# Performance work log

Hardware: AMD Instinct MI355X
Metric: run time of the kernel (lower is better)

The kernel has to match this reference:

```python
import jax, jax.numpy as jnp
import numpy as np

B, N, OUTERDIM, DIM, N_CLASSES = 2, 6000, 1024, 512, 2
HEADS, DIM_HEAD, INNER = 8, 64, 512
LANDMARKS, PINV_ITERS, KPAD = 256, 6, 16  # residual conv kernel 33 -> pad 16
SCALE = DIM_HEAD ** -0.5


def layer_norm(x, g, b, eps=1e-5):
    mu = x.mean(-1, keepdims=True)
    var = jnp.var(x, axis=-1, keepdims=True)
    return (x - mu) * jax.lax.rsqrt(var + eps) * g + b


def moore_penrose_pinv(x, iters=PINV_ITERS):
    # x: [b, h, m, m]
    abs_x = jnp.abs(x)
    col = abs_x.sum(-1)
    row = abs_x.sum(-2)
    z = jnp.swapaxes(x, -1, -2) / (jnp.max(col) * jnp.max(row))
    I = jnp.eye(x.shape[-1], dtype=x.dtype)
    for _ in range(iters):
        xz = x @ z
        z = 0.25 * z @ (13 * I - xz @ (15 * I - xz @ (7 * I - xz)))
    return z


def nystrom_attention(x, w_qkv, w_out, b_out, conv_w):
    b, n, _ = x.shape
    pad = (-n) % LANDMARKS
    xp = jnp.pad(x, ((0, 0), (pad, 0), (0, 0)))  # pad at FRONT, as in lucidrains impl
    npad = n + pad
    qkv = xp @ w_qkv.T  # [b, npad, 3*inner]
    q, k, v = [t.reshape(b, npad, HEADS, DIM_HEAD).transpose(0, 2, 1, 3)
               for t in jnp.split(qkv, 3, axis=-1)]
    q = q * SCALE
    l = npad // LANDMARKS  # tokens per landmark
    q_l = q.reshape(b, HEADS, LANDMARKS, l, DIM_HEAD).sum(3) / l
    k_l = k.reshape(b, HEADS, LANDMARKS, l, DIM_HEAD).sum(3) / l
    attn1 = jax.nn.softmax(jnp.einsum('bhid,bhjd->bhij', q, k_l), axis=-1)   # [b,h,npad,m]
    attn2 = jax.nn.softmax(jnp.einsum('bhid,bhjd->bhij', q_l, k_l), axis=-1)  # [b,h,m,m]
    attn3 = jax.nn.softmax(jnp.einsum('bhid,bhjd->bhij', q_l, k), axis=-1)    # [b,h,m,npad]
    out = (attn1 @ moore_penrose_pinv(attn2)) @ (attn3 @ v)  # [b,h,npad,d]
    # depthwise residual conv over sequence dim (per head), kernel (33,1)
    out = out + jax.lax.conv_general_dilated(
        v, conv_w, window_strides=(1, 1), padding=((KPAD, KPAD), (0, 0)),
        dimension_numbers=('NCHW', 'OIHW', 'NCHW'), feature_group_count=HEADS)
    out = out.transpose(0, 2, 1, 3).reshape(b, npad, INNER)
    out = out @ w_out.T + b_out
    return out[:, -n:]


def setup_inputs() -> dict:
    key = jax.random.key(0)
    ks = jax.random.split(key, 12)
    w = lambda k, shape: 0.02 * jax.random.normal(k, shape, dtype=jnp.float32)
    inp = {
        'data': jax.random.normal(ks[0], (B, N, OUTERDIM), dtype=jnp.float32),
        'w1': w(ks[1], (DIM, OUTERDIM)), 'b1': jnp.zeros((DIM,), jnp.float32),
        'cls_token': jax.random.normal(ks[2], (1, 1, DIM), dtype=jnp.float32),
        'ln1_g': jnp.ones((DIM,), jnp.float32), 'ln1_b': jnp.zeros((DIM,), jnp.float32),
        'qkv1_w': w(ks[3], (3 * INNER, DIM)),
        'out1_w': w(ks[4], (DIM, INNER)), 'out1_b': jnp.zeros((DIM,), jnp.float32),
        'conv1_w': w(ks[5], (HEADS, 1, 33, 1)),
        'ln2_g': jnp.ones((DIM,), jnp.float32), 'ln2_b': jnp.zeros((DIM,), jnp.float32),
        'qkv2_w': w(ks[6], (3 * INNER, DIM)),
        'out2_w': w(ks[7], (DIM, INNER)), 'out2_b': jnp.zeros((DIM,), jnp.float32),
        'conv2_w': w(ks[8], (HEADS, 1, 33, 1)),
        'lnf_g': jnp.ones((DIM,), jnp.float32), 'lnf_b': jnp.zeros((DIM,), jnp.float32),
        'w2': w(ks[9], (N_CLASSES, DIM)), 'b2': jnp.zeros((N_CLASSES,), jnp.float32),
    }
    return inp


def reference(data, w1, b1, cls_token, ln1_g, ln1_b, qkv1_w, out1_w, out1_b, conv1_w,
              ln2_g, ln2_b, qkv2_w, out2_w, out2_b, conv2_w, lnf_g, lnf_b, w2, b2):
    h = jax.nn.relu(data @ w1.T + b1)  # [B, N, DIM]
    H = h.shape[1]
    side = int(np.ceil(np.sqrt(H)))
    add = side * side - H
    h = jnp.concatenate([h, h[:, :add]], axis=1)  # square padding: 6084
    cls = jnp.broadcast_to(cls_token, (h.shape[0], 1, h.shape[2]))
    h = jnp.concatenate([cls, h], axis=1)  # +CLS: 6085
    h = h + nystrom_attention(layer_norm(h, ln1_g, ln1_b), qkv1_w, out1_w, out1_b, conv1_w)
    h = h + nystrom_attention(layer_norm(h, ln2_g, ln2_b), qkv2_w, out2_w, out2_b, conv2_w)
    h = layer_norm(h, lnf_g, lnf_b)[:, 0]
    logits = h @ w2.T + b2
    return logits
```

## Files before the change

kernel.cpp:

```cpp
#include <hip/hip_runtime.h>
#include <cstdint>
#include <cstddef>

namespace {

constexpr int DIMC  = 512;
constexpr int SEQ   = 6085;
constexpr int NPAD  = 6144;
constexpr int PADF  = 59;
constexpr int LMK   = 256;
constexpr int BHN   = 16;
constexpr int KSPL  = 16;
constexpr int MPADR = 6016;

typedef __attribute__((ext_vector_type(8))) short bf8_t;
typedef __attribute__((ext_vector_type(4))) float f4_t;

#define SWZB(r, cu) (((((r) << 6) + ((cu) << 1))) ^ (((r) & 7) << 4))

#define GLDS16(gp, lp) __builtin_amdgcn_global_load_lds( \
    (const __attribute__((address_space(1))) void*)(gp), \
    (__attribute__((address_space(3))) void*)(lp), 16, 0, 0)

__device__ __forceinline__ ushort f2bf(float f) {
    union { float f; uint32_t u; } c{f};
    uint32_t u = c.u;
    return (ushort)((u + 0x7FFFu + ((u >> 16) & 1u)) >> 16);
}
__device__ __forceinline__ float bf2f(ushort u) {
    union { uint32_t u; float f; } c{(uint32_t)u << 16};
    return c.f;
}

__device__ __forceinline__ float waveSum(float v) {
#pragma unroll
    for (int o = 32; o > 0; o >>= 1) v += __shfl_xor(v, o, 64);
    return v;
}
__device__ __forceinline__ float waveMax(float v) {
#pragma unroll
    for (int o = 32; o > 0; o >>= 1) v = fmaxf(v, __shfl_xor(v, o, 64));
    return v;
}
__device__ __forceinline__ float blockSum256(float v, float* sm) {
    v = waveSum(v);
    __syncthreads();
    if ((threadIdx.x & 63) == 0) sm[threadIdx.x >> 6] = v;
    __syncthreads();
    return sm[0] + sm[1] + sm[2] + sm[3];
}
__device__ __forceinline__ float blockMax256(float v, float* sm) {
    v = waveMax(v);
    __syncthreads();
    if ((threadIdx.x & 63) == 0) sm[threadIdx.x >> 6] = v;
    __syncthreads();
    return fmaxf(fmaxf(sm[0], sm[1]), fmaxf(sm[2], sm[3]));
}

template<int EPI>
__global__ __launch_bounds__(256)
void gemm_bt(const ushort* __restrict__ A, const ushort* __restrict__ B,
             void* __restrict__ Cv, int M, int N, int K,
             int lda, int ldb, int ldc,
             long long sA, long long sB, long long sC,
             const float* __restrict__ bias, int relu,
             ushort* __restrict__ qp, ushort* __restrict__ kp, ushort* __restrict__ vp)
{
    __shared__ __align__(16) char As_s[128 * 128];
    __shared__ __align__(16) char Bs_s[128 * 128];
    const int z = blockIdx.z;
    const ushort* Ab = A + (size_t)z * sA;
    const ushort* Bb = B + (size_t)z * sB;
    const int row0 = blockIdx.y * 128, col0 = blockIdx.x * 128;
    const int tid = threadIdx.x, wid = tid >> 6, lane = tid & 63;
    const int wr = wid >> 1, wc = wid & 1, lr = lane & 15, kg = lane >> 4;
    const int srow = lane >> 3, sq = lane & 7;
    f4_t acc[4][4] = {};
    for (int k0 = 0; k0 < K; k0 += 64) {
        __syncthreads();
#pragma unroll
        for (int i = 0; i < 4; ++i) {
            int r = wid * 32 + i * 8 + srow;
            int qs = sq ^ (r & 7);
            GLDS16(Ab + (size_t)(row0 + r) * lda + k0 + qs * 8,
                   As_s + (wid * 32 + i * 8) * 128);
        }
#pragma unroll
        for (int i = 0; i < 4; ++i) {
            int r = wid * 32 + i * 8 + srow;
            int qs = sq ^ (r & 7);
            GLDS16(Bb + (size_t)(col0 + r) * ldb + k0 + qs * 8,
                   Bs_s + (wid * 32 + i * 8) * 128);
        }
        asm volatile("s_waitcnt vmcnt(0)" ::: "memory");
        __syncthreads();
#pragma unroll
        for (int ks = 0; ks < 2; ++ks) {
            bf8_t af[4], bg[4];
#pragma unroll
            for (int mr = 0; mr < 4; ++mr) {
                int r = wr * 64 + mr * 16 + lr;
                af[mr] = *(const bf8_t*)(As_s + r * 128 + ((((ks << 2) | kg) ^ (r & 7)) << 4));
            }
#pragma unroll
            for (int nr = 0; nr < 4; ++nr) {
                int r = wc * 64 + nr * 16 + lr;
                bg[nr] = *(const bf8_t*)(Bs_s + r * 128 + ((((ks << 2) | kg) ^ (r & 7)) << 4));
            }
#pragma unroll
            for (int mr = 0; mr < 4; ++mr)
#pragma unroll
                for (int nr = 0; nr < 4; ++nr)
                    acc[mr][nr] = __builtin_amdgcn_mfma_f32_16x16x32_bf16(af[mr], bg[nr], acc[mr][nr], 0, 0, 0);
        }
    }
#pragma unroll
    for (int mr = 0; mr < 4; ++mr) {
#pragma unroll
        for (int nr = 0; nr < 4; ++nr) {
#pragma unroll
            for (int r = 0; r < 4; ++r) {
                int gm = row0 + wr * 64 + mr * 16 + kg * 4 + r;
                int gn = col0 + wc * 64 + nr * 16 + lr;
                if (gm >= M || gn >= N) continue;
                float val = acc[mr][nr][r];
                if (EPI == 0) {
                    if (bias) val += bias[gn];
                    if (relu) val = fmaxf(val, 0.f);
                    ((float*)Cv)[(size_t)z * sC + (size_t)gm * ldc + gn] = val;
                } else if (EPI == 1) {
                    ((ushort*)Cv)[(size_t)z * sC + (size_t)gm * ldc + gn] = f2bf(val);
                } else {
                    int b = (gm >= NPAD) ? 1 : 0;
                    int i = gm - b * NPAD;
                    int which = gn >> 9, hh = (gn >> 6) & 7, d = gn & 63;
                    size_t dst = ((size_t)(b * 8 + hh) * NPAD + i) * 64 + d;
                    if (which == 0)      qp[dst] = f2bf(val * 0.125f);
                    else if (which == 1) kp[dst] = f2bf(val);
                    else                 vp[dst] = f2bf(val);
                }
            }
        }
    }
}

__global__ __launch_bounds__(256)
void attn1_fused(const ushort* __restrict__ q, const ushort* __restrict__ kl,
                 const ushort* __restrict__ Wt, ushort* __restrict__ ot)
{
    __shared__ __align__(16) char P_s[128 * 512];
    const int mt = blockIdx.x;
    const int bh = blockIdx.y;
    const int b = bh >> 3, hh = bh & 7;
    const int tid = threadIdx.x, wid = tid >> 6, lane = tid & 63;
    const int lr = lane & 15, kg = lane >> 4;
    const int row0 = mt * 128;
    const ushort* qb  = q  + (size_t)bh * NPAD * 64;
    const ushort* klb = kl + (size_t)bh * LMK * 64;
    const ushort* Wtb = Wt + (size_t)bh * 128 * 256;

    f4_t acc[2][16];
#pragma unroll
    for (int mf = 0; mf < 2; ++mf)
#pragma unroll
        for (int nf = 0; nf < 16; ++nf) acc[mf][nf] = (f4_t){0.f, 0.f, 0.f, 0.f};
#pragma unroll
    for (int ks = 0; ks < 2; ++ks) {
        bf8_t af[2];
#pragma unroll
        for (int mf = 0; mf < 2; ++mf)
            af[mf] = *(const bf8_t*)&qb[(size_t)(row0 + wid * 32 + mf * 16 + lr) * 64 + ks * 32 + kg * 8];
#pragma unroll
        for (int nf = 0; nf < 16; ++nf) {
            bf8_t bg = *(const bf8_t*)&klb[(size_t)(nf * 16 + lr) * 64 + ks * 32 + kg * 8];
            acc[0][nf] = __builtin_amdgcn_mfma_f32_16x16x32_bf16(af[0], bg, acc[0][nf], 0, 0, 0);
            acc[1][nf] = __builtin_amdgcn_mfma_f32_16x16x32_bf16(af[1], bg, acc[1][nf], 0, 0, 0);
        }
    }
    float inv_s[2][4];
#pragma unroll
    for (int mf = 0; mf < 2; ++mf) {
        float mx[4] = {-1e30f, -1e30f, -1e30f, -1e30f};
#pragma unroll
        for (int nf = 0; nf < 16; ++nf)
#pragma unroll
            for (int r = 0; r < 4; ++r) mx[r] = fmaxf(mx[r], acc[mf][nf][r]);
#pragma unroll
        for (int r = 0; r < 4; ++r) {
            mx[r] = fmaxf(mx[r], __shfl_xor(mx[r], 1, 64));
            mx[r] = fmaxf(mx[r], __shfl_xor(mx[r], 2, 64));
            mx[r] = fmaxf(mx[r], __shfl_xor(mx[r], 4, 64));
            mx[r] = fmaxf(mx[r], __shfl_xor(mx[r], 8, 64));
        }
        float sum[4] = {0.f, 0.f, 0.f, 0.f};
        const int rowb = wid * 32 + mf * 16 + kg * 4;
        const int cc2 = (lr & 7) * 2;
        const int chi = lr >> 3;
#pragma unroll
        for (int nf = 0; nf < 16; ++nf) {
#pragma unroll
            for (int r = 0; r < 4; ++r) {
                float e = expf(acc[mf][nf][r] - mx[r]);
                sum[r] += e;
                int row = rowb + r;
                int chunk = (2 * nf + chi) ^ (row & 7);
                *(ushort*)(P_s + row * 512 + chunk * 16 + cc2) = f2bf(e);
            }
        }
#pragma unroll
        for (int r = 0; r < 4; ++r) {
            sum[r] += __shfl_xor(sum[r], 1, 64);
            sum[r] += __shfl_xor(sum[r], 2, 64);
            sum[r] += __shfl_xor(sum[r], 4, 64);
            sum[r] += __shfl_xor(sum[r], 8, 64);
            inv_s[mf][r] = 1.f / sum[r];
        }
    }
    f4_t acc2[2][4] = {};
#pragma unroll
    for (int kt = 0; kt < 8; ++kt) {
        bf8_t af2[2];
#pragma unroll
        for (int mf = 0; mf < 2; ++mf) {
            int row = wid * 32 + mf * 16 + lr;
            int chunk = (kt * 4 + kg) ^ (row & 7);
            af2[mf] = *(const bf8_t*)(P_s + row * 512 + chunk * 16);
        }
#pragma unroll
        for (int nf = 0; nf < 4; ++nf) {
            bf8_t bg = *(const bf8_t*)&Wtb[(size_t)(nf * 16 + lr) * 256 + kt * 32 + kg * 8];
            acc2[0][nf] = __builtin_amdgcn_mfma_f32_16x16x32_bf16(af2[0], bg, acc2[0][nf], 0, 0, 0);
            acc2[1][nf] = __builtin_amdgcn_mfma_f32_16x16x32_bf16(af2[1], bg, acc2[1][nf], 0, 0, 0);
        }
    }
#pragma unroll
    for (int mf = 0; mf < 2; ++mf)
#pragma unroll
        for (int nf = 0; nf < 4; ++nf)
#pragma unroll
            for (int r = 0; r < 4; ++r) {
                int gm = row0 + wid * 32 + mf * 16 + kg * 4 + r;
                int gn = nf * 16 + lr;
                ot[((size_t)(b * NPAD + gm)) * DIMC + hh * 64 + gn] =
                    f2bf(acc2[mf][nf][r] * inv_s[mf][r]);
            }
}

__global__ __launch_bounds__(256)
void gemm_ns(const ushort* __restrict__ A, const ushort* __restrict__ B,
             ushort* __restrict__ C, ushort* __restrict__ C2, ushort* __restrict__ CT,
             float alpha, float c2d, int K, int N,
             long long sA, long long sB, long long sC, long long sCT)
{
    __shared__ __align__(16) char As_s[64 * 64];
    __shared__ __align__(16) char Bs_s[64 * 64];
    const int z = blockIdx.z;
    const int row0 = blockIdx.y * 64, col0 = blockIdx.x * 64;
    const int tid = threadIdx.x;
    const int wid = tid >> 6, lane = tid & 63;
    const int lr = lane & 15, kg = lane >> 4;
    const ushort* Ab = A + (size_t)z * sA;
    const ushort* Bb = B + (size_t)z * sB;
    f4_t acc[4] = {};
    const int am = tid >> 2, ac8 = (tid & 3) * 8;
    for (int k0 = 0; k0 < K; k0 += 32) {
        *(bf8_t*)(As_s + SWZB(am, ac8)) = *(const bf8_t*)&Ab[(size_t)(row0 + am) * K + k0 + ac8];
#pragma unroll
        for (int p = 0; p < 8; ++p) {
            int kk = p * 4 + (tid >> 6), n = tid & 63;
            *(ushort*)(Bs_s + SWZB(n, kk)) = Bb[(size_t)(k0 + kk) * N + col0 + n];
        }
        __syncthreads();
        bf8_t af = *(const bf8_t*)(As_s + SWZB(wid * 16 + lr, kg * 8));
#pragma unroll
        for (int j = 0; j < 4; ++j) {
            bf8_t bg = *(const bf8_t*)(Bs_s + SWZB(j * 16 + lr, kg * 8));
            acc[j] = __builtin_amdgcn_mfma_f32_16x16x32_bf16(af, bg, acc[j], 0, 0, 0);
        }
        __syncthreads();
    }
#pragma unroll
    for (int j = 0; j < 4; ++j) {
#pragma unroll
        for (int r = 0; r < 4; ++r) {
            int gm = row0 + wid * 16 + kg * 4 + r;
            int gn = col0 + j * 16 + lr;
            float val = alpha * acc[j][r];
            if (C)  C[(size_t)z * sC + (size_t)gm * N + gn] = f2bf(val);
            if (C2) C2[(size_t)z * sC + (size_t)gm * N + gn] = f2bf(((gm == gn) ? c2d : 0.f) - val);
            if (CT) CT[(size_t)z * sCT + (size_t)gn * LMK + gm] = f2bf(val);
        }
    }
}

__global__ __launch_bounds__(256)
void pv_splitk(const ushort* __restrict__ S, const ushort* __restrict__ v,
               float* __restrict__ o2p)
{
    __shared__ __align__(16) char As_s[128 * 64];
    __shared__ __align__(16) char Bs_s[64 * 64];
    const int split = blockIdx.x, mt = blockIdx.y, bh = blockIdx.z;
    const int tid = threadIdx.x;
    const int wid = tid >> 6, lane = tid & 63;
    const int lr = lane & 15, kg = lane >> 4;
    const ushort* Sb = S + (size_t)bh * LMK * NPAD + (size_t)(mt * 128) * NPAD;
    const ushort* vb = v + (size_t)bh * NPAD * 64;
    const int ks0 = split * (NPAD / KSPL);
    f4_t acc[2][4] = {};
    for (int k0 = ks0; k0 < ks0 + NPAD / KSPL; k0 += 32) {
#pragma unroll
        for (int p = 0; p < 2; ++p) {
            int idx = p * 256 + tid;
            int m = idx >> 2, kc = (idx & 3) * 8;
            *(bf8_t*)(As_s + SWZB(m, kc)) = *(const bf8_t*)&Sb[(size_t)m * NPAD + k0 + kc];
        }
#pragma unroll
        for (int p = 0; p < 8; ++p) {
            int kk = p * 4 + (tid >> 6), n = tid & 63;
            *(ushort*)(Bs_s + SWZB(n, kk)) = vb[(size_t)(k0 + kk) * 64 + n];
        }
        __syncthreads();
        bf8_t af[2], bg[4];
#pragma unroll
        for (int i = 0; i < 2; ++i)
            af[i] = *(const bf8_t*)(As_s + SWZB(wid * 32 + i * 16 + lr, kg * 8));
#pragma unroll
        for (int j = 0; j < 4; ++j)
            bg[j] = *(const bf8_t*)(Bs_s + SWZB(j * 16 + lr, kg * 8));
#pragma unroll
        for (int i = 0; i < 2; ++i)
#pragma unroll
            for (int j = 0; j < 4; ++j)
                acc[i][j] = __builtin_amdgcn_mfma_f32_16x16x32_bf16(af[i], bg[j], acc[i][j], 0, 0, 0);
        __syncthreads();
    }
#pragma unroll
    for (int i = 0; i < 2; ++i)
#pragma unroll
        for (int j = 0; j < 4; ++j)
#pragma unroll
            for (int r = 0; r < 4; ++r) {
                int gm = mt * 128 + wid * 32 + i * 16 + kg * 4 + r;
                int gn = j * 16 + lr;
                o2p[((size_t)(split * BHN + bh) * LMK + gm) * 64 + gn] = acc[i][j][r];
            }
}

__global__ void reduce_o2(const float* __restrict__ o2p, ushort* __restrict__ o2) {
    int idx = blockIdx.x * 256 + threadIdx.x;
    int bh = idx >> 14, e = idx & 16383;
    float s = 0.f;
#pragma unroll
    for (int sp = 0; sp < KSPL; ++sp)
        s += o2p[((size_t)(sp * BHN + bh) << 14) + e];
    o2[idx] = f2bf(s);
}

__global__ void cvt_bf16(const float* __restrict__ in, ushort* __restrict__ out, int n8) {
    int i = blockIdx.x * 256 + threadIdx.x;
    if (i >= n8) return;
    float4 a = ((const float4*)in)[i * 2], b = ((const float4*)in)[i * 2 + 1];
    ushort4 lo = { f2bf(a.x), f2bf(a.y), f2bf(a.z), f2bf(a.w) };
    ushort4 hi = { f2bf(b.x), f2bf(b.y), f2bf(b.z), f2bf(b.w) };
    ((ushort4*)out)[i * 2] = lo;
    ((ushort4*)out)[i * 2 + 1] = hi;
}

__global__ void extend_h(float* __restrict__ h, const float* __restrict__ cls) {
    int b = blockIdx.y, bx = blockIdx.x;
    float* hb = h + (size_t)b * SEQ * DIMC;
    for (int c = threadIdx.x; c < DIMC; c += 256) {
        if (bx == 0) hb[c] = cls[c];
        else hb[(size_t)(6000 + bx) * DIMC + c] = hb[(size_t)bx * DIMC + c];
    }
}

__global__ void zero_xp_pad(ushort* __restrict__ xp) {
    int e = blockIdx.x * 256 + threadIdx.x;
    int b = e / (PADF * DIMC);
    int rest = e - b * (PADF * DIMC);
    xp[(size_t)b * NPAD * DIMC + rest] = 0;
}

__global__ __launch_bounds__(128)
void ln_to_xp(const float* __restrict__ h, const float* __restrict__ g,
              const float* __restrict__ bb, ushort* __restrict__ xp)
{
    __shared__ float sm[2];
    int r = blockIdx.x;
    int b = r / SEQ, i = r - b * SEQ;
    int t = threadIdx.x;
    const float4* row = (const float4*)(h + (size_t)r * DIMC);
    float4 x = row[t];
    float s  = x.x + x.y + x.z + x.w;
    float sq = x.x * x.x + x.y * x.y + x.z * x.z + x.w * x.w;
    s = waveSum(s);
    sq = waveSum(sq);
    int w = t >> 6;
    if ((t & 63) == 0) sm[w] = s;
    __syncthreads();
    float S = sm[0] + sm[1];
    __syncthreads();
    if ((t & 63) == 0) sm[w] = sq;
    __syncthreads();
    float SQ = sm[0] + sm[1];
    float mu = S * (1.f / DIMC);
    float var = SQ * (1.f / DIMC) - mu * mu;
    float rs = rsqrtf(var + 1e-5f);
    float4 gg = ((const float4*)g)[t];
    float4 bv = ((const float4*)bb)[t];
    ushort4 o;
    o.x = f2bf((x.x - mu) * rs * gg.x + bv.x);
    o.y = f2bf((x.y - mu) * rs * gg.y + bv.y);
    o.z = f2bf((x.z - mu) * rs * gg.z + bv.z);
    o.w = f2bf((x.w - mu) * rs * gg.w + bv.w);
    ((ushort4*)(xp + ((size_t)b * NPAD + PADF + i) * DIMC))[t] = o;
}

__global__ void landmark_mean(const ushort* __restrict__ in, ushort* __restrict__ out) {
    int m = blockIdx.x, bh = blockIdx.y, d = threadIdx.x;
    const ushort* p = in + ((size_t)bh * NPAD + (size_t)m * (NPAD / LMK)) * 64 + d;
    float s = 0.f;
#pragma unroll
    for (int j = 0; j < NPAD / LMK; ++j) s += bf2f(p[(size_t)j * 64]);
    out[((size_t)bh * LMK + m) * 64 + d] = f2bf(s * (1.f / (NPAD / LMK)));
}

__global__ __launch_bounds__(256)
void softmax_bf_wide(ushort* __restrict__ S) {
    __shared__ float sm[4];
    ushort* p = S + (size_t)blockIdx.x * NPAD;
    int t = threadIdx.x;
    float v[24];
    float mx = -1e30f;
#pragma unroll
    for (int j = 0; j < 24; ++j) { v[j] = bf2f(p[j * 256 + t]); mx = fmaxf(mx, v[j]); }
    float bm = blockMax256(mx, sm);
    float s = 0.f;
#pragma unroll
    for (int j = 0; j < 24; ++j) { v[j] = expf(v[j] - bm); s += v[j]; }
    float bs = blockSum256(s, sm);
    float inv = 1.f / bs;
#pragma unroll
    for (int j = 0; j < 24; ++j) p[j * 256 + t] = f2bf(v[j] * inv);
}

__global__ __launch_bounds__(256)
void softmax_bf256(ushort* __restrict__ S) {
    __shared__ float sm[4];
    ushort* p = S + (size_t)blockIdx.x * 256;
    int t = threadIdx.x;
    float v = bf2f(p[t]);
    float bm = blockMax256(v, sm);
    float e = expf(v - bm);
    float bs = blockSum256(e, sm);
    p[t] = f2bf(e / bs);
}

__global__ __launch_bounds__(256)
void colsum_max(const ushort* __restrict__ X, float* __restrict__ scal) {
    __shared__ float sm[4];
    int bh = blockIdx.x, t = threadIdx.x;
    const ushort* Xb = X + ((size_t)bh << 16);
    float s = 0.f;
#pragma unroll 8
    for (int i = 0; i < 256; ++i) s += bf2f(Xb[(size_t)i * 256 + t]);
    float m = blockMax256(s, sm);
    if (t == 0) atomicMax((unsigned int*)scal, __float_as_uint(m));
}

__global__ void init_z(const ushort* __restrict__ X, const float* __restrict__ scal,
                       ushort* __restrict__ Z) {
    size_t e = (size_t)blockIdx.x * 256 + threadIdx.x;
    int c = (int)(e & 255);
    int r = (int)((e >> 8) & 255);
    size_t bh = e >> 16;
    float inv = 1.f / scal[0];
    Z[e] = f2bf(bf2f(X[(bh << 16) + (size_t)c * 256 + r]) * inv);
}

__global__ __launch_bounds__(256)
void conv_add(const ushort* __restrict__ v, const float* __restrict__ cw,
              ushort* __restrict__ ot)
{
    __shared__ float w[33];
    __shared__ ushort vt[96][64];
    int bh = blockIdx.y;
    int b = bh >> 3, hh = bh & 7;
    int i0 = blockIdx.x * 64;
    int t = threadIdx.x;
    if (t < 33) w[t] = cw[hh * 33 + t];
    const ushort* vb = v + (size_t)bh * NPAD * 64;
    int d = t & 63;
    for (int rr = t >> 6; rr < 96; rr += 4) {
        int j = i0 - 16 + rr;
        vt[rr][d] = (j >= 0 && j < NPAD) ? vb[(size_t)j * 64 + d] : (ushort)0;
    }
    __syncthreads();
    for (int ii = t >> 6; ii < 64; ii += 4) {
        float acc = 0.f;
#pragma unroll
        for (int kk = 0; kk < 33; ++kk) acc += w[kk] * bf2f(vt[ii + kk][d]);
        size_t off = ((size_t)(b * NPAD + i0 + ii)) * DIMC + hh * 64 + d;
        ot[off] = f2bf(bf2f(ot[off]) + acc);
    }
}

__global__ void residual_add(float* __restrict__ h, const float* __restrict__ y) {
    size_t e = (size_t)blockIdx.x * 256 + threadIdx.x;
    int c = (int)(e & 511);
    size_t ri = e >> 9;
    int i = (int)(ri % SEQ);
    int b = (int)(ri / SEQ);
    h[e] += y[((size_t)b * NPAD + PADF + i) * DIMC + c];
}

__global__ __launch_bounds__(256)
void final_head(const float* __restrict__ h, const float* __restrict__ g,
                const float* __restrict__ bb, const float* __restrict__ w2,
                const float* __restrict__ b2, float* __restrict__ out)
{
    __shared__ float row[DIMC];
    __shared__ float sm[4];
    int b = blockIdx.x;
    int t = threadIdx.x;
    const float* x = h + (size_t)b * SEQ * DIMC;
    float v0 = x[t], v1 = x[t + 256];
    float S = blockSum256(v0 + v1, sm);
    float SQ = blockSum256(v0 * v0 + v1 * v1, sm);
    float mu = S * (1.f / DIMC);
    float rs = rsqrtf(SQ * (1.f / DIMC) - mu * mu + 1e-5f);
    row[t] = (v0 - mu) * rs * g[t] + bb[t];
    row[t + 256] = (v1 - mu) * rs * g[t + 256] + bb[t + 256];
    __syncthreads();
    if (t < 64) {
        float a0 = 0.f, a1 = 0.f;
        for (int idx = t; idx < DIMC; idx += 64) {
            a0 += row[idx] * w2[idx];
            a1 += row[idx] * w2[DIMC + idx];
        }
        a0 = waveSum(a0);
        a1 = waveSum(a1);
        if (t == 0) {
            out[b * 2 + 0] = a0 + b2[0];
            out[b * 2 + 1] = a1 + b2[1];
        }
    }
}

void bt(int epi, const ushort* A, const ushort* B, void* C, int M, int N, int K,
        int lda, int ldb, int ldc, long long sA, long long sB, long long sC, int batch,
        const float* bias, int relu, ushort* qp, ushort* kp, ushort* vp, hipStream_t s)
{
    dim3 g((N + 127) / 128, (M + 127) / 128, batch), blk(256);
    switch (epi) {
    case 0: gemm_bt<0><<<g, blk, 0, s>>>(A, B, C, M, N, K, lda, ldb, ldc, sA, sB, sC, bias, relu, qp, kp, vp); break;
    case 1: gemm_bt<1><<<g, blk, 0, s>>>(A, B, C, M, N, K, lda, ldb, ldc, sA, sB, sC, bias, relu, qp, kp, vp); break;
    default: gemm_bt<2><<<g, blk, 0, s>>>(A, B, C, M, N, K, lda, ldb, ldc, sA, sB, sC, bias, relu, qp, kp, vp); break;
    }
}

void ns(const ushort* A, const ushort* B, ushort* C, ushort* C2, ushort* CT,
        float alpha, float c2d, int M, int N, int K,
        long long sA, long long sB, long long sC, long long sCT, hipStream_t s)
{
    dim3 g(N / 64, M / 64, BHN), blk(256);
    gemm_ns<<<g, blk, 0, s>>>(A, B, C, C2, CT, alpha, c2d, K, N, sA, sB, sC, sCT);
}

struct WS {
    float *h, *scal, *o2p, *y;
    ushort *xp, *q, *k, *v, *ql, *kl;
    ushort *datab, *w1b, *qkvwb1, *qkvwb2, *outwb1, *outwb2;
    ushort *X, *Z0, *Z1, *XZ, *TA, *TB, *TC;
    ushort *o2b, *Wt, *S, *ot;
};

void nystrom_layer(float* h, const float* lng, const float* lnb,
                   const ushort* qkvwb, const ushort* outwb, const float* outb,
                   const float* convw, const WS& w, hipStream_t s)
{
    const long long SM = (long long)LMK * LMK;
    zero_xp_pad<<<(2 * PADF * DIMC) / 256, 256, 0, s>>>(w.xp);
    ln_to_xp<<<2 * SEQ, 128, 0, s>>>(h, lng, lnb, w.xp);
    bt(2, w.xp, qkvwb, nullptr, 2 * NPAD, 3 * DIMC, DIMC, DIMC, DIMC, 0,
       0, 0, 0, 1, nullptr, 0, w.q, w.k, w.v, s);
    landmark_mean<<<dim3(LMK, BHN), 64, 0, s>>>(w.q, w.ql);
    landmark_mean<<<dim3(LMK, BHN), 64, 0, s>>>(w.k, w.kl);
    bt(1, w.ql, w.kl, w.X, LMK, LMK, 64, 64, 64, LMK,
       (long long)LMK * 64, (long long)LMK * 64, SM, BHN, nullptr, 0, nullptr, nullptr, nullptr, s);
    softmax_bf256<<<BHN * LMK, 256, 0, s>>>(w.X);
    hipMemsetAsync(w.scal, 0, 8, s);
    colsum_max<<<BHN, 256, 0, s>>>(w.X, w.scal);
    init_z<<<(BHN * LMK * LMK) / 256, 256, 0, s>>>(w.X, w.scal, w.Z0);
    ushort* Zc = w.Z0;
    ushort* Zn = w.Z1;
    for (int it = 0; it < 6; ++it) {
        ns(w.X, Zc, w.XZ, w.TA, nullptr, 1.f, 7.f, LMK, LMK, LMK, SM, SM, SM, 0, s);
        ns(w.XZ, w.TA, w.TB, w.TC, nullptr, 1.f, 15.f, LMK, LMK, LMK, SM, SM, SM, 0, s);
        ns(w.XZ, w.TC, w.TB, w.TA, nullptr, 1.f, 13.f, LMK, LMK, LMK, SM, SM, SM, 0, s);
        ns(Zc, w.TA, Zn, nullptr, nullptr, 0.25f, 0.f, LMK, LMK, LMK, SM, SM, SM, 0, s);
        ushort* t = Zc; Zc = Zn; Zn = t;
    }
    bt(1, w.ql, w.k, w.S, LMK, NPAD, 64, 64, 64, NPAD,
       (long long)LMK * 64, (long long)NPAD * 64, (long long)LMK * NPAD, BHN,
       nullptr, 0, nullptr, nullptr, nullptr, s);
    softmax_bf_wide<<<BHN * LMK, 256, 0, s>>>(w.S);
    pv_splitk<<<dim3(KSPL, 2, BHN), 256, 0, s>>>(w.S, w.v, w.o2p);
    reduce_o2<<<BHN * LMK * 64 / 256, 256, 0, s>>>(w.o2p, w.o2b);
    ns(Zc, w.o2b, nullptr, nullptr, w.Wt, 1.f, 0.f, LMK, 64, LMK,
       SM, (long long)LMK * 64, 0, 128 * 256, s);
    attn1_fused<<<dim3(NPAD / 128, BHN), 256, 0, s>>>(w.q, w.kl, w.Wt, w.ot);
    conv_add<<<dim3(NPAD / 64, BHN), 256, 0, s>>>(w.v, convw, w.ot);
    bt(0, w.ot, outwb, w.y, 2 * NPAD, DIMC, DIMC, DIMC, DIMC, DIMC,
       0, 0, 0, 1, outb, 0, nullptr, nullptr, nullptr, s);
    residual_add<<<(2 * SEQ * DIMC) / 256, 256, 0, s>>>(h, w.y);
}

}

extern "C" void kernel_launch(void* const* d_in, const int* in_sizes, int n_in,
                              void* d_out, int out_size, void* d_ws, size_t ws_size,
                              hipStream_t stream)
{
    (void)in_sizes; (void)n_in; (void)out_size;
    const float* data  = (const float*)d_in[0];
    const float* w1    = (const float*)d_in[1];
    const float* b1    = (const float*)d_in[2];
    const float* cls   = (const float*)d_in[3];
    const float* ln1g  = (const float*)d_in[4];
    const float* ln1b  = (const float*)d_in[5];
    const float* qkv1w = (const float*)d_in[6];
    const float* out1w = (const float*)d_in[7];
    const float* out1b = (const float*)d_in[8];
    const float* conv1 = (const float*)d_in[9];
    const float* ln2g  = (const float*)d_in[10];
    const float* ln2b  = (const float*)d_in[11];
    const float* qkv2w = (const float*)d_in[12];
    const float* out2w = (const float*)d_in[13];
    const float* out2b = (const float*)d_in[14];
    const float* conv2 = (const float*)d_in[15];
    const float* lnfg  = (const float*)d_in[16];
    const float* lnfb  = (const float*)d_in[17];
    const float* w2    = (const float*)d_in[18];
    const float* b2    = (const float*)d_in[19];
    float* out = (float*)d_out;

    if (ws_size < 209473792ull) return;
    char* p = (char*)d_ws;
    auto alloc = [&](size_t bytes) { char* r = p; p += (bytes + 255) & ~(size_t)255; return r; };
    WS w;
    w.h     = (float*)alloc((size_t)2 * SEQ * DIMC * 4);
    w.xp    = (ushort*)alloc((size_t)2 * NPAD * DIMC * 2);
    w.q     = (ushort*)alloc((size_t)BHN * NPAD * 64 * 2);
    w.k     = (ushort*)alloc((size_t)BHN * NPAD * 64 * 2);
    w.v     = (ushort*)alloc((size_t)BHN * NPAD * 64 * 2);
    w.ql    = (ushort*)alloc((size_t)BHN * LMK * 64 * 2);
    w.kl    = (ushort*)alloc((size_t)BHN * LMK * 64 * 2);
    w.scal  = (float*)alloc(256);
    w.datab = (ushort*)alloc((size_t)2 * MPADR * 1024 * 2);
    w.w1b   = (ushort*)alloc((size_t)512 * 1024 * 2);
    w.qkvwb1= (ushort*)alloc((size_t)1536 * 512 * 2);
    w.qkvwb2= (ushort*)alloc((size_t)1536 * 512 * 2);
    w.outwb1= (ushort*)alloc((size_t)512 * 512 * 2);
    w.outwb2= (ushort*)alloc((size_t)512 * 512 * 2);
    w.X     = (ushort*)alloc((size_t)BHN * LMK * LMK * 2);
    w.Z0    = (ushort*)alloc((size_t)BHN * LMK * LMK * 2);
    w.Z1    = (ushort*)alloc((size_t)BHN * LMK * LMK * 2);
    w.XZ    = (ushort*)alloc((size_t)BHN * LMK * LMK * 2);
    w.TA    = (ushort*)alloc((size_t)BHN * LMK * LMK * 2);
    w.TB    = (ushort*)alloc((size_t)BHN * LMK * LMK * 2);
    w.TC    = (ushort*)alloc((size_t)BHN * LMK * LMK * 2);
    w.o2p   = (float*)alloc((size_t)KSPL * BHN * LMK * 64 * 4);
    w.o2b   = (ushort*)alloc((size_t)BHN * LMK * 64 * 2);
    w.Wt    = (ushort*)alloc((size_t)BHN * 128 * 256 * 2);
    w.S     = (ushort*)alloc((size_t)BHN * LMK * NPAD * 2);
    w.y     = (float*)w.S;
    w.ot    = w.k;

    for (int b = 0; b < 2; ++b)
        cvt_bf16<<<3000, 256, 0, stream>>>(data + (size_t)b * 6000 * 1024,
                                           w.datab + (size_t)b * MPADR * 1024, 768000);
    cvt_bf16<<<256, 256, 0, stream>>>(w1, w.w1b, 65536);
    cvt_bf16<<<384, 256, 0, stream>>>(qkv1w, w.qkvwb1, 98304);
    cvt_bf16<<<384, 256, 0, stream>>>(qkv2w, w.qkvwb2, 98304);
    cvt_bf16<<<128, 256, 0, stream>>>(out1w, w.outwb1, 32768);
    cvt_bf16<<<128, 256, 0, stream>>>(out2w, w.outwb2, 32768);

    bt(0, w.datab, w.w1b, w.h + DIMC, 6000, DIMC, 1024, 1024, 1024, DIMC,
       (long long)MPADR * 1024, 0, (long long)SEQ * DIMC, 2, b1, 1,
       nullptr, nullptr, nullptr, stream);
    extend_h<<<dim3(85, 2), 256, 0, stream>>>(w.h, cls);

    nystrom_layer(w.h, ln1g, ln1b, w.qkvwb1, w.outwb1, out1b, conv1, w, stream);
    nystrom_layer(w.h, ln2g, ln2b, w.qkvwb2, w.outwb2, out2b, conv2, w, stream);

    final_head<<<2, 256, 0, stream>>>(w.h, lnfg, lnfb, w2, b2, out);
}
```

Baseline: 1.019 ms.

## Fuse landmark-to-token attention into flash-style split-K kernel with transposed V

Replaces the separate QK^T GEMM, wide softmax over a 256x6144 score matrix, and split-K PV GEMM with a single online-softmax kernel that keeps scores in LDS and writes per-split max/sum for a rescaling reduction. V is stored transposed by the QKV GEMM epilogue, so both the PV step and the conv read contiguous rows. attn1_fused is retiled to 64-row blocks for more blocks and less LDS per block, and expf is swapped for __expf. This drops a large intermediate score tensor round-trip through memory, at the cost of strided scattered writes of vT in the GEMM epilogue and slightly lower exp precision.

```diff
diff --git a/kernel.cpp b/kernel.cpp
--- a/kernel.cpp
+++ b/kernel.cpp
@@ -16,6 +16,8 @@
 typedef __attribute__((ext_vector_type(8))) short bf8_t;
 typedef __attribute__((ext_vector_type(4))) float f4_t;
 
+#define MFMA(a, b, c) __builtin_amdgcn_mfma_f32_16x16x32_bf16(a, b, c, 0, 0, 0)
+
 #define SWZB(r, cu) (((((r) << 6) + ((cu) << 1))) ^ (((r) & 7) << 4))
 
 #define GLDS16(gp, lp) __builtin_amdgcn_global_load_lds( \
@@ -55,6 +57,20 @@
     if ((threadIdx.x & 63) == 0) sm[threadIdx.x >> 6] = v;
     __syncthreads();
     return fmaxf(fmaxf(sm[0], sm[1]), fmaxf(sm[2], sm[3]));
+}
+__device__ __forceinline__ float grpMax(float v) {
+    v = fmaxf(v, __shfl_xor(v, 1, 64));
+    v = fmaxf(v, __shfl_xor(v, 2, 64));
+    v = fmaxf(v, __shfl_xor(v, 4, 64));
+    v = fmaxf(v, __shfl_xor(v, 8, 64));
+    return v;
+}
+__device__ __forceinline__ float grpSum(float v) {
+    v += __shfl_xor(v, 1, 64);
+    v += __shfl_xor(v, 2, 64);
+    v += __shfl_xor(v, 4, 64);
+    v += __shfl_xor(v, 8, 64);
+    return v;
 }
 
 template<int EPI>
@@ -111,7 +127,7 @@
             for (int mr = 0; mr < 4; ++mr)
 #pragma unroll
                 for (int nr = 0; nr < 4; ++nr)
-                    acc[mr][nr] = __builtin_amdgcn_mfma_f32_16x16x32_bf16(af[mr], bg[nr], acc[mr][nr], 0, 0, 0);
+                    acc[mr][nr] = MFMA(af[mr], bg[nr], acc[mr][nr]);
         }
     }
 #pragma unroll
@@ -134,116 +150,218 @@
                     int b = (gm >= NPAD) ? 1 : 0;
                     int i = gm - b * NPAD;
                     int which = gn >> 9, hh = (gn >> 6) & 7, d = gn & 63;
-                    size_t dst = ((size_t)(b * 8 + hh) * NPAD + i) * 64 + d;
-                    if (which == 0)      qp[dst] = f2bf(val * 0.125f);
-                    else if (which == 1) kp[dst] = f2bf(val);
-                    else                 vp[dst] = f2bf(val);
+                    if (which == 0)
+                        qp[((size_t)(b * 8 + hh) * NPAD + i) * 64 + d] = f2bf(val * 0.125f);
+                    else if (which == 1)
+                        kp[((size_t)(b * 8 + hh) * NPAD + i) * 64 + d] = f2bf(val);
+                    else
+                        vp[((size_t)(b * 8 + hh) * 64 + d) * NPAD + i] = f2bf(val);
                 }
             }
         }
     }
+}
+
+__global__ __launch_bounds__(256)
+void pv_flash(const ushort* __restrict__ ql, const ushort* __restrict__ k,
+              const ushort* __restrict__ vT, float* __restrict__ o2p,
+              float* __restrict__ lmb, float* __restrict__ lsb)
+{
+    __shared__ __align__(16) char P_s[128 * 256];
+    const int split = blockIdx.x, mt = blockIdx.y, bh = blockIdx.z;
+    const int tid = threadIdx.x, wid = tid >> 6, lane = tid & 63;
+    const int lr = lane & 15, kg = lane >> 4;
+    const int rowb = wid * 32;
+    const ushort* qlb = ql + ((size_t)bh * LMK + mt * 128) * 64;
+    const ushort* kb  = k  + (size_t)bh * NPAD * 64;
+    const ushort* vTb = vT + (size_t)bh * 64 * NPAD;
+    const int kv0 = split * (NPAD / KSPL);
+
+    float mrun[2][4], lrun[2][4];
+    f4_t acco[2][4] = {};
+#pragma unroll
+    for (int mf = 0; mf < 2; ++mf)
+#pragma unroll
+        for (int r = 0; r < 4; ++r) { mrun[mf][r] = -3.0e38f; lrun[mf][r] = 0.f; }
+
+    for (int kvt = 0; kvt < 3; ++kvt) {
+        const int kvb = kv0 + kvt * 128;
+        f4_t sacc[2][8] = {};
+#pragma unroll
+        for (int ks = 0; ks < 2; ++ks) {
+            bf8_t af[2];
+#pragma unroll
+            for (int mf = 0; mf < 2; ++mf)
+                af[mf] = *(const bf8_t*)&qlb[(size_t)(rowb + mf * 16 + lr) * 64 + ks * 32 + kg * 8];
+#pragma unroll
+            for (int nf = 0; nf < 8; ++nf) {
+                bf8_t bg = *(const bf8_t*)&kb[(size_t)(kvb + nf * 16 + lr) * 64 + ks * 32 + kg * 8];
+                sacc[0][nf] = MFMA(af[0], bg, sacc[0][nf]);
+                sacc[1][nf] = MFMA(af[1], bg, sacc[1][nf]);
+            }
+        }
+#pragma unroll
+        for (int mf = 0; mf < 2; ++mf) {
+            float tmax[4] = {-3.0e38f, -3.0e38f, -3.0e38f, -3.0e38f};
+#pragma unroll
+            for (int nf = 0; nf < 8; ++nf)
+#pragma unroll
+                for (int r = 0; r < 4; ++r) tmax[r] = fmaxf(tmax[r], sacc[mf][nf][r]);
+#pragma unroll
+            for (int r = 0; r < 4; ++r) {
+                tmax[r] = grpMax(tmax[r]);
+                float mnew = fmaxf(mrun[mf][r], tmax[r]);
+                float sc = __expf(mrun[mf][r] - mnew);
+                mrun[mf][r] = mnew;
+                lrun[mf][r] *= sc;
+#pragma unroll
+                for (int nf2 = 0; nf2 < 4; ++nf2) acco[mf][nf2][r] *= sc;
+            }
+            float lsum[4] = {0.f, 0.f, 0.f, 0.f};
+            const int rb2 = rowb + mf * 16 + kg * 4;
+            const int cc2 = (lr & 7) * 2, chi = lr >> 3;
+#pragma unroll
+            for (int nf = 0; nf < 8; ++nf)
+#pragma unroll
+                for (int r = 0; r < 4; ++r) {
+                    float e = __expf(sacc[mf][nf][r] - mrun[mf][r]);
+                    lsum[r] += e;
+                    int row = rb2 + r;
+                    int chunk = (2 * nf + chi) ^ (row & 7);
+                    *(ushort*)(P_s + row * 256 + chunk * 16 + cc2) = f2bf(e);
+                }
+#pragma unroll
+            for (int r = 0; r < 4; ++r) lrun[mf][r] += grpSum(lsum[r]);
+        }
+#pragma unroll
+        for (int kt2 = 0; kt2 < 4; ++kt2) {
+            bf8_t af2[2];
+#pragma unroll
+            for (int mf = 0; mf < 2; ++mf) {
+                int row = rowb + mf * 16 + lr;
+                int chunk = (kt2 * 4 + kg) ^ (row & 7);
+                af2[mf] = *(const bf8_t*)(P_s + row * 256 + chunk * 16);
+            }
+#pragma unroll
+            for (int nf2 = 0; nf2 < 4; ++nf2) {
+                bf8_t bg = *(const bf8_t*)&vTb[(size_t)(nf2 * 16 + lr) * NPAD + kvb + kt2 * 32 + kg * 8];
+                acco[0][nf2] = MFMA(af2[0], bg, acco[0][nf2]);
+                acco[1][nf2] = MFMA(af2[1], bg, acco[1][nf2]);
+            }
+        }
+    }
+#pragma unroll
+    for (int mf = 0; mf < 2; ++mf)
+#pragma unroll
+        for (int nf2 = 0; nf2 < 4; ++nf2)
+#pragma unroll
+            for (int r = 0; r < 4; ++r) {
+                int gm = mt * 128 + rowb + mf * 16 + kg * 4 + r;
+                o2p[((size_t)(split * BHN + bh) * LMK + gm) * 64 + nf2 * 16 + lr] = acco[mf][nf2][r];
+            }
+    if (lr == 0) {
+#pragma unroll
+        for (int mf = 0; mf < 2; ++mf)
+#pragma unroll
+            for (int r = 0; r < 4; ++r) {
+                int gm = mt * 128 + rowb + mf * 16 + kg * 4 + r;
+                lmb[(size_t)(split * BHN + bh) * LMK + gm] = mrun[mf][r];
+                lsb[(size_t)(split * BHN + bh) * LMK + gm] = lrun[mf][r];
+            }
+    }
+}
+
+__global__ void reduce_o2(const float* __restrict__ o2p, const float* __restrict__ lmb,
+                          const float* __restrict__ lsb, ushort* __restrict__ o2)
+{
+    int idx = blockIdx.x * 256 + threadIdx.x;
+    int bh = idx >> 14, m = (idx >> 6) & 255, d = idx & 63;
+    float gm = -3.0e38f;
+#pragma unroll
+    for (int s = 0; s < KSPL; ++s)
+        gm = fmaxf(gm, lmb[(size_t)(s * BHN + bh) * LMK + m]);
+    float num = 0.f, den = 0.f;
+#pragma unroll
+    for (int s = 0; s < KSPL; ++s) {
+        float wgt = __expf(lmb[(size_t)(s * BHN + bh) * LMK + m] - gm);
+        num += wgt * o2p[((size_t)(s * BHN + bh) * LMK + m) * 64 + d];
+        den += wgt * lsb[(size_t)(s * BHN + bh) * LMK + m];
+    }
+    o2[idx] = f2bf(num / den);
 }
 
 __global__ __launch_bounds__(256)
 void attn1_fused(const ushort* __restrict__ q, const ushort* __restrict__ kl,
                  const ushort* __restrict__ Wt, ushort* __restrict__ ot)
 {
-    __shared__ __align__(16) char P_s[128 * 512];
+    __shared__ __align__(16) char P_s[64 * 512];
     const int mt = blockIdx.x;
     const int bh = blockIdx.y;
     const int b = bh >> 3, hh = bh & 7;
     const int tid = threadIdx.x, wid = tid >> 6, lane = tid & 63;
     const int lr = lane & 15, kg = lane >> 4;
-    const int row0 = mt * 128;
+    const int row0 = mt * 64, rowb = wid * 16;
     const ushort* qb  = q  + (size_t)bh * NPAD * 64;
     const ushort* klb = kl + (size_t)bh * LMK * 64;
     const ushort* Wtb = Wt + (size_t)bh * 128 * 256;
 
-    f4_t acc[2][16];
-#pragma unroll
-    for (int mf = 0; mf < 2; ++mf)
-#pragma unroll
-        for (int nf = 0; nf < 16; ++nf) acc[mf][nf] = (f4_t){0.f, 0.f, 0.f, 0.f};
+    f4_t acc[16];
+#pragma unroll
+    for (int nf = 0; nf < 16; ++nf) acc[nf] = (f4_t){0.f, 0.f, 0.f, 0.f};
 #pragma unroll
     for (int ks = 0; ks < 2; ++ks) {
-        bf8_t af[2];
-#pragma unroll
-        for (int mf = 0; mf < 2; ++mf)
-            af[mf] = *(const bf8_t*)&qb[(size_t)(row0 + wid * 32 + mf * 16 + lr) * 64 + ks * 32 + kg * 8];
+        bf8_t af = *(const bf8_t*)&qb[(size_t)(row0 + rowb + lr) * 64 + ks * 32 + kg * 8];
 #pragma unroll
         for (int nf = 0; nf < 16; ++nf) {
             bf8_t bg = *(const bf8_t*)&klb[(size_t)(nf * 16 + lr) * 64 + ks * 32 + kg * 8];
-            acc[0][nf] = __builtin_amdgcn_mfma_f32_16x16x32_bf16(af[0], bg, acc[0][nf], 0, 0, 0);
-            acc[1][nf] = __builtin_amdgcn_mfma_f32_16x16x32_bf16(af[1], bg, acc[1][nf], 0, 0, 0);
-        }
-    }
-    float inv_s[2][4];
-#pragma unroll
-    for (int mf = 0; mf < 2; ++mf) {
-        float mx[4] = {-1e30f, -1e30f, -1e30f, -1e30f};
+            acc[nf] = MFMA(af, bg, acc[nf]);
+        }
+    }
+    float inv_s[4];
+    {
+        float mx[4] = {-3.0e38f, -3.0e38f, -3.0e38f, -3.0e38f};
 #pragma unroll
         for (int nf = 0; nf < 16; ++nf)
 #pragma unroll
-            for (int r = 0; r < 4; ++r) mx[r] = fmaxf(mx[r], acc[mf][nf][r]);
-#pragma unroll
-        for (int r = 0; r < 4; ++r) {
-            mx[r] = fmaxf(mx[r], __shfl_xor(mx[r], 1, 64));
-            mx[r] = fmaxf(mx[r], __shfl_xor(mx[r], 2, 64));
-            mx[r] = fmaxf(mx[r], __shfl_xor(mx[r], 4, 64));
-            mx[r] = fmaxf(mx[r], __shfl_xor(mx[r], 8, 64));
-        }
+            for (int r = 0; r < 4; ++r) mx[r] = fmaxf(mx[r], acc[nf][r]);
+#pragma unroll
+        for (int r = 0; r < 4; ++r) mx[r] = grpMax(mx[r]);
         float sum[4] = {0.f, 0.f, 0.f, 0.f};
-        const int rowb = wid * 32 + mf * 16 + kg * 4;
-        const int cc2 = (lr & 7) * 2;
-        const int chi = lr >> 3;
-#pragma unroll
-        for (int nf = 0; nf < 16; ++nf) {
+        const int rb2 = rowb + kg * 4;
+        const int cc2 = (lr & 7) * 2, chi = lr >> 3;
+#pragma unroll
+        for (int nf = 0; nf < 16; ++nf)
 #pragma unroll
             for (int r = 0; r < 4; ++r) {
-                float e = expf(acc[mf][nf][r] - mx[r]);
+                float e = __expf(acc[nf][r] - mx[r]);
                 sum[r] += e;
-                int row = rowb + r;
+                int row = rb2 + r;
                 int chunk = (2 * nf + chi) ^ (row & 7);
                 *(ushort*)(P_s + row * 512 + chunk * 16 + cc2) = f2bf(e);
             }
-        }
-#pragma unroll
-        for (int r = 0; r < 4; ++r) {
-            sum[r] += __shfl_xor(sum[r], 1, 64);
-            sum[r] += __shfl_xor(sum[r], 2, 64);
-            sum[r] += __shfl_xor(sum[r], 4, 64);
-            sum[r] += __shfl_xor(sum[r], 8, 64);
-            inv_s[mf][r] = 1.f / sum[r];
-        }
-    }
-    f4_t acc2[2][4] = {};
+#pragma unroll
+        for (int r = 0; r < 4; ++r) inv_s[r] = 1.f / grpSum(sum[r]);
+    }
+    f4_t acc2[4] = {};
 #pragma unroll
     for (int kt = 0; kt < 8; ++kt) {
-        bf8_t af2[2];
-#pragma unroll
-        for (int mf = 0; mf < 2; ++mf) {
-            int row = wid * 32 + mf * 16 + lr;
-            int chunk = (kt * 4 + kg) ^ (row & 7);
-            af2[mf] = *(const bf8_t*)(P_s + row * 512 + chunk * 16);
-        }
+        int row = rowb + lr;
+        int chunk = (kt * 4 + kg) ^ (row & 7);
+        bf8_t af2 = *(const bf8_t*)(P_s + row * 512 + chunk * 16);
 #pragma unroll
         for (int nf = 0; nf < 4; ++nf) {
             bf8_t bg = *(const bf8_t*)&Wtb[(size_t)(nf * 16 + lr) * 256 + kt * 32 + kg * 8];
-            acc2[0][nf] = __builtin_amdgcn_mfma_f32_16x16x32_bf16(af2[0], bg, acc2[0][nf], 0, 0, 0);
-            acc2[1][nf] = __builtin_amdgcn_mfma_f32_16x16x32_bf16(af2[1], bg, acc2[1][nf], 0, 0, 0);
-        }
-    }
-#pragma unroll
-    for (int mf = 0; mf < 2; ++mf)
-#pragma unroll
-        for (int nf = 0; nf < 4; ++nf)
-#pragma unroll
-            for (int r = 0; r < 4; ++r) {
-                int gm = row0 + wid * 32 + mf * 16 + kg * 4 + r;
-                int gn = nf * 16 + lr;
-                ot[((size_t)(b * NPAD + gm)) * DIMC + hh * 64 + gn] =
-                    f2bf(acc2[mf][nf][r] * inv_s[mf][r]);
-            }
+            acc2[nf] = MFMA(af2, bg, acc2[nf]);
+        }
+    }
+#pragma unroll
+    for (int nf = 0; nf < 4; ++nf)
+#pragma unroll
+        for (int r = 0; r < 4; ++r) {
+            int gm = row0 + rowb + kg * 4 + r;
+            int gn = nf * 16 + lr;
+            ot[((size_t)(b * NPAD + gm)) * DIMC + hh * 64 + gn] = f2bf(acc2[nf][r] * inv_s[r]);
+        }
 }
 
 __global__ __launch_bounds__(256)
@@ -275,7 +393,7 @@
 #pragma unroll
         for (int j = 0; j < 4; ++j) {
             bf8_t bg = *(const bf8_t*)(Bs_s + SWZB(j * 16 + lr, kg * 8));
-            acc[j] = __builtin_amdgcn_mfma_f32_16x16x32_bf16(af, bg, acc[j], 0, 0, 0);
+            acc[j] = MFMA(af, bg, acc[j]);
         }
         __syncthreads();
     }
@@ -291,69 +409,6 @@
             if (CT) CT[(size_t)z * sCT + (size_t)gn * LMK + gm] = f2bf(val);
         }
     }
-}
-
-__global__ __launch_bounds__(256)
-void pv_splitk(const ushort* __restrict__ S, const ushort* __restrict__ v,
-               float* __restrict__ o2p)
-{
-    __shared__ __align__(16) char As_s[128 * 64];
-    __shared__ __align__(16) char Bs_s[64 * 64];
-    const int split = blockIdx.x, mt = blockIdx.y, bh = blockIdx.z;
-    const int tid = threadIdx.x;
-    const int wid = tid >> 6, lane = tid & 63;
-    const int lr = lane & 15, kg = lane >> 4;
-    const ushort* Sb = S + (size_t)bh * LMK * NPAD + (size_t)(mt * 128) * NPAD;
-    const ushort* vb = v + (size_t)bh * NPAD * 64;
-    const int ks0 = split * (NPAD / KSPL);
-    f4_t acc[2][4] = {};
-    for (int k0 = ks0; k0 < ks0 + NPAD / KSPL; k0 += 32) {
-#pragma unroll
-        for (int p = 0; p < 2; ++p) {
-            int idx = p * 256 + tid;
-            int m = idx >> 2, kc = (idx & 3) * 8;
-            *(bf8_t*)(As_s + SWZB(m, kc)) = *(const bf8_t*)&Sb[(size_t)m * NPAD + k0 + kc];
-        }
-#pragma unroll
-        for (int p = 0; p < 8; ++p) {
-            int kk = p * 4 + (tid >> 6), n = tid & 63;
-            *(ushort*)(Bs_s + SWZB(n, kk)) = vb[(size_t)(k0 + kk) * 64 + n];
-        }
-        __syncthreads();
-        bf8_t af[2], bg[4];
-#pragma unroll
-        for (int i = 0; i < 2; ++i)
-            af[i] = *(const bf8_t*)(As_s + SWZB(wid * 32 + i * 16 + lr, kg * 8));
-#pragma unroll
-        for (int j = 0; j < 4; ++j)
-            bg[j] = *(const bf8_t*)(Bs_s + SWZB(j * 16 + lr, kg * 8));
-#pragma unroll
-        for (int i = 0; i < 2; ++i)
-#pragma unroll
-            for (int j = 0; j < 4; ++j)
-                acc[i][j] = __builtin_amdgcn_mfma_f32_16x16x32_bf16(af[i], bg[j], acc[i][j], 0, 0, 0);
-        __syncthreads();
-    }
-#pragma unroll
-    for (int i = 0; i < 2; ++i)
-#pragma unroll
-        for (int j = 0; j < 4; ++j)
-#pragma unroll
-            for (int r = 0; r < 4; ++r) {
-                int gm = mt * 128 + wid * 32 + i * 16 + kg * 4 + r;
-                int gn = j * 16 + lr;
-                o2p[((size_t)(split * BHN + bh) * LMK + gm) * 64 + gn] = acc[i][j][r];
-            }
-}
-
-__global__ void reduce_o2(const float* __restrict__ o2p, ushort* __restrict__ o2) {
-    int idx = blockIdx.x * 256 + threadIdx.x;
-    int bh = idx >> 14, e = idx & 16383;
-    float s = 0.f;
-#pragma unroll
-    for (int sp = 0; sp < KSPL; ++sp)
-        s += o2p[((size_t)(sp * BHN + bh) << 14) + e];
-    o2[idx] = f2bf(s);
 }
 
 __global__ void cvt_bf16(const float* __restrict__ in, ushort* __restrict__ out, int n8) {
@@ -427,32 +482,13 @@
 }
 
 __global__ __launch_bounds__(256)
-void softmax_bf_wide(ushort* __restrict__ S) {
-    __shared__ float sm[4];
-    ushort* p = S + (size_t)blockIdx.x * NPAD;
-    int t = threadIdx.x;
-    float v[24];
-    float mx = -1e30f;
-#pragma unroll
-    for (int j = 0; j < 24; ++j) { v[j] = bf2f(p[j * 256 + t]); mx = fmaxf(mx, v[j]); }
-    float bm = blockMax256(mx, sm);
-    float s = 0.f;
-#pragma unroll
-    for (int j = 0; j < 24; ++j) { v[j] = expf(v[j] - bm); s += v[j]; }
-    float bs = blockSum256(s, sm);
-    float inv = 1.f / bs;
-#pragma unroll
-    for (int j = 0; j < 24; ++j) p[j * 256 + t] = f2bf(v[j] * inv);
-}
-
-__global__ __launch_bounds__(256)
 void softmax_bf256(ushort* __restrict__ S) {
     __shared__ float sm[4];
     ushort* p = S + (size_t)blockIdx.x * 256;
     int t = threadIdx.x;
     float v = bf2f(p[t]);
     float bm = blockMax256(v, sm);
-    float e = expf(v - bm);
+    float e = __expf(v - bm);
     float bs = blockSum256(e, sm);
     p[t] = f2bf(e / bs);
 }
@@ -480,27 +516,28 @@
 }
 
 __global__ __launch_bounds__(256)
-void conv_add(const ushort* __restrict__ v, const float* __restrict__ cw,
+void conv_add(const ushort* __restrict__ vT, const float* __restrict__ cw,
               ushort* __restrict__ ot)
 {
     __shared__ float w[33];
-    __shared__ ushort vt[96][64];
+    __shared__ ushort vt[64][97];
     int bh = blockIdx.y;
     int b = bh >> 3, hh = bh & 7;
     int i0 = blockIdx.x * 64;
     int t = threadIdx.x;
     if (t < 33) w[t] = cw[hh * 33 + t];
-    const ushort* vb = v + (size_t)bh * NPAD * 64;
+    const ushort* vTb = vT + (size_t)bh * 64 * NPAD;
+    for (int idx = t; idx < 64 * 96; idx += 256) {
+        int d = idx / 96, jj = idx - d * 96;
+        int j = i0 - 16 + jj;
+        vt[d][jj] = (j >= 0 && j < NPAD) ? vTb[(size_t)d * NPAD + j] : (ushort)0;
+    }
+    __syncthreads();
     int d = t & 63;
-    for (int rr = t >> 6; rr < 96; rr += 4) {
-        int j = i0 - 16 + rr;
-        vt[rr][d] = (j >= 0 && j < NPAD) ? vb[(size_t)j * 64 + d] : (ushort)0;
-    }
-    __syncthreads();
     for (int ii = t >> 6; ii < 64; ii += 4) {
         float acc = 0.f;
 #pragma unroll
-        for (int kk = 0; kk < 33; ++kk) acc += w[kk] * bf2f(vt[ii + kk][d]);
+        for (int kk = 0; kk < 33; ++kk) acc += w[kk] * bf2f(vt[d][ii + kk]);
         size_t off = ((size_t)(b * NPAD + i0 + ii)) * DIMC + hh * 64 + d;
         ot[off] = f2bf(bf2f(ot[off]) + acc);
     }
@@ -569,8 +606,8 @@
 }
 
 struct WS {
-    float *h, *scal, *o2p, *y;
-    ushort *xp, *q, *k, *v, *ql, *kl;
+    float *h, *scal, *o2p, *y, *lmb, *lsb;
+    ushort *xp, *q, *k, *vT, *ql, *kl;
     ushort *datab, *w1b, *qkvwb1, *qkvwb2, *outwb1, *outwb2;
     ushort *X, *Z0, *Z1, *XZ, *TA, *TB, *TC;
     ushort *o2b, *Wt, *S, *ot;
@@ -584,7 +621,7 @@
     zero_xp_pad<<<(2 * PADF * DIMC) / 256, 256, 0, s>>>(w.xp);
     ln_to_xp<<<2 * SEQ, 128, 0, s>>>(h, lng, lnb, w.xp);
     bt(2, w.xp, qkvwb, nullptr, 2 * NPAD, 3 * DIMC, DIMC, DIMC, DIMC, 0,
-       0, 0, 0, 1, nullptr, 0, w.q, w.k, w.v, s);
+       0, 0, 0, 1, nullptr, 0, w.q, w.k, w.vT, s);
     landmark_mean<<<dim3(LMK, BHN), 64, 0, s>>>(w.q, w.ql);
     landmark_mean<<<dim3(LMK, BHN), 64, 0, s>>>(w.k, w.kl);
     bt(1, w.ql, w.kl, w.X, LMK, LMK, 64, 64, 64, LMK,
@@ -602,16 +639,12 @@
         ns(Zc, w.TA, Zn, nullptr, nullptr, 0.25f, 0.f, LMK, LMK, LMK, SM, SM, SM, 0, s);
         ushort* t = Zc; Zc = Zn; Zn = t;
     }
-    bt(1, w.ql, w.k, w.S, LMK, NPAD, 64, 64, 64, NPAD,
-       (long long)LMK * 64, (long long)NPAD * 64, (long long)LMK * NPAD, BHN,
-       nullptr, 0, nullptr, nullptr, nullptr, s);
-    softmax_bf_wide<<<BHN * LMK, 256, 0, s>>>(w.S);
-    pv_splitk<<<dim3(KSPL, 2, BHN), 256, 0, s>>>(w.S, w.v, w.o2p);
-    reduce_o2<<<BHN * LMK * 64 / 256, 256, 0, s>>>(w.o2p, w.o2b);
+    pv_flash<<<dim3(KSPL, 2, BHN), 256, 0, s>>>(w.ql, w.k, w.vT, w.o2p, w.lmb, w.lsb);
+    reduce_o2<<<BHN * LMK * 64 / 256, 256, 0, s>>>(w.o2p, w.lmb, w.lsb, w.o2b);
     ns(Zc, w.o2b, nullptr, nullptr, w.Wt, 1.f, 0.f, LMK, 64, LMK,
        SM, (long long)LMK * 64, 0, 128 * 256, s);
-    attn1_fused<<<dim3(NPAD / 128, BHN), 256, 0, s>>>(w.q, w.kl, w.Wt, w.ot);
-    conv_add<<<dim3(NPAD / 64, BHN), 256, 0, s>>>(w.v, convw, w.ot);
+    attn1_fused<<<dim3(NPAD / 64, BHN), 256, 0, s>>>(w.q, w.kl, w.Wt, w.ot);
+    conv_add<<<dim3(NPAD / 64, BHN), 256, 0, s>>>(w.vT, convw, w.ot);
     bt(0, w.ot, outwb, w.y, 2 * NPAD, DIMC, DIMC, DIMC, DIMC, DIMC,
        0, 0, 0, 1, outb, 0, nullptr, nullptr, nullptr, s);
     residual_add<<<(2 * SEQ * DIMC) / 256, 256, 0, s>>>(h, w.y);
@@ -654,7 +687,7 @@
     w.xp    = (ushort*)alloc((size_t)2 * NPAD * DIMC * 2);
     w.q     = (ushort*)alloc((size_t)BHN * NPAD * 64 * 2);
     w.k     = (ushort*)alloc((size_t)BHN * NPAD * 64 * 2);
-    w.v     = (ushort*)alloc((size_t)BHN * NPAD * 64 * 2);
+    w.vT    = (ushort*)alloc((size_t)BHN * 64 * NPAD * 2);
     w.ql    = (ushort*)alloc((size_t)BHN * LMK * 64 * 2);
     w.kl    = (ushort*)alloc((size_t)BHN * LMK * 64 * 2);
     w.scal  = (float*)alloc(256);
@@ -672,6 +705,8 @@
     w.TB    = (ushort*)alloc((size_t)BHN * LMK * LMK * 2);
     w.TC    = (ushort*)alloc((size_t)BHN * LMK * LMK * 2);
     w.o2p   = (float*)alloc((size_t)KSPL * BHN * LMK * 64 * 4);
+    w.lmb   = (float*)alloc((size_t)KSPL * BHN * LMK * 4);
+    w.lsb   = (float*)alloc((size_t)KSPL * BHN * LMK * 4);
     w.o2b   = (ushort*)alloc((size_t)BHN * LMK * 64 * 2);
     w.Wt    = (ushort*)alloc((size_t)BHN * 128 * 256 * 2);
     w.S     = (ushort*)alloc((size_t)BHN * LMK * NPAD * 2);
```

Measured after the change: 1.094 ms. +7.4%, slower.
